# Kernel tuning notes

Measured on AMD Instinct MI355X. Metric: run time of the kernel, lower is better.

## Reference

```python
import jax, jax.numpy as jnp
import numpy as np

D = 256  # subgraph_width
N_CLASSES = 10
EPS = 1e-5  # torch LayerNorm default


def _layernorm(x, g, b):
    mu = jnp.mean(x, axis=-1, keepdims=True)
    var = jnp.var(x, axis=-1, keepdims=True)
    return (x - mu) * jax.lax.rsqrt(var + EPS) * g + b


def setup_inputs() -> dict:
    key = jax.random.key(0)
    ks = jax.random.split(key, 16)
    B, T, N = 64, 512, 512
    traj = jax.random.normal(ks[0], (B, T, 2), dtype=jnp.float32)
    labels = jax.random.randint(ks[1], (B,), 0, N_CLASSES)
    h = jax.random.normal(ks[2], (B, N, D), dtype=jnp.float32)
    valid_len = jnp.maximum(jax.random.randint(ks[3], (B,), 0, N), 1)
    s = 0.02
    params = dict(
        emb=jax.random.normal(ks[4], (N_CLASSES, D), dtype=jnp.float32) * s,
        w_mlp=jax.random.normal(ks[5], (2, D), dtype=jnp.float32) * s,
        b_mlp=jnp.zeros((D,), jnp.float32),
        ln_g=jnp.ones((D,), jnp.float32),
        ln_b=jnp.zeros((D,), jnp.float32),
        wq=jax.random.normal(ks[6], (D, D), dtype=jnp.float32) * s,
        bq=jnp.zeros((D,), jnp.float32),
        wk=jax.random.normal(ks[7], (D, D), dtype=jnp.float32) * s,
        bk=jnp.zeros((D,), jnp.float32),
        wv=jax.random.normal(ks[8], (D, D), dtype=jnp.float32) * s,
        bv=jnp.zeros((D,), jnp.float32),
        w_out=jax.random.normal(ks[9], (D, 1), dtype=jnp.float32) * s,
        b_out=jnp.zeros((1,), jnp.float32),
    )
    return dict(traj=traj, labels=labels, h=h, valid_len=valid_len, **params)


def reference(traj, labels, h, valid_len, emb, w_mlp, b_mlp, ln_g, ln_b,
              wq, bq, wk, bk, wv, bv, w_out, b_out):
    # MLP(in=2, out=D, activation='leaky'): Linear -> LayerNorm -> LeakyReLU
    x = jax.nn.leaky_relu(_layernorm(traj @ w_mlp + b_mlp, ln_g, ln_b))  # [B,T,D]
    le = emb[labels]                          # [B,D]
    x = x + le[:, None, :]                    # embed-add
    # SelfAttentionWithKeyFCLayer: Q from x, K/V from h, scaled, key-masked by valid_len
    q = x @ wq + bq                            # [B,T,D]
    k = h @ wk + bk                            # [B,N,D]
    v = h @ wv + bv                            # [B,N,D]
    scores = jnp.einsum('btd,bnd->btn', q, k) / jnp.sqrt(jnp.float32(D))
    N = h.shape[1]
    key_mask = jnp.arange(N)[None, :] < valid_len[:, None]          # [B,N]
    scores = jnp.where(key_mask[:, None, :], scores, jnp.float32(-1e9))
    attn = jax.nn.softmax(scores, axis=-1)
    enc = jnp.einsum('btn,bnd->btd', attn, v)  # [B,T,D]
    pooled = jnp.max(enc, axis=1) + le          # [B,D]
    return jax.nn.sigmoid(pooled @ w_out + b_out)  # [B,1]
```

## Files before the change

### kernel.cpp

```cpp
#include <hip/hip_runtime.h>
#include <math.h>

typedef float f32x4 __attribute__((ext_vector_type(4)));
typedef __bf16 bf16x8 __attribute__((ext_vector_type(8)));
typedef unsigned short u16x8 __attribute__((ext_vector_type(8)));
typedef unsigned short u16x4 __attribute__((ext_vector_type(4)));
typedef unsigned int u32x4 __attribute__((ext_vector_type(4)));

#define MFMA(a, b, c) __builtin_amdgcn_mfma_f32_16x16x32_bf16((a), (b), (c), 0, 0, 0)

static __device__ __forceinline__ unsigned short f2bf(float f) {
  unsigned u = __float_as_uint(f);
  u += 0x7FFFu + ((u >> 16) & 1u);
  return (unsigned short)(u >> 16);
}
static __device__ __forceinline__ float bf2f(unsigned short s) {
  return __uint_as_float(((unsigned)s) << 16);
}
static __device__ __forceinline__ unsigned pack2bf(float lo, float hi) {
  return (unsigned)f2bf(lo) | ((unsigned)f2bf(hi) << 16);
}

static __device__ __forceinline__ int swz512(int row, int col) {
  return row * 512 + (col ^ ((((row & 7) ^ (col >> 6)) & 7) << 4));
}
static __device__ __forceinline__ int swzV(int d, int col) {
  return d * 64 + (col ^ (((d >> 1) & 3) << 4));
}
static __device__ __forceinline__ int swzO(int d, int col) {
  return d * 256 + (col ^ ((((d & 7) ^ (col >> 7)) & 7) << 4));
}

static __device__ __forceinline__ void barp() {
  __builtin_amdgcn_sched_barrier(0);
  asm volatile("s_waitcnt lgkmcnt(0)");
  __builtin_amdgcn_s_barrier();
  __builtin_amdgcn_sched_barrier(0);
}

__global__ __launch_bounds__(256) void setup(
    const float* __restrict__ w0m, const float* __restrict__ w1m, const float* __restrict__ w2m,
    unsigned short* __restrict__ t0m, unsigned short* __restrict__ t1m, unsigned short* __restrict__ t2m,
    const float* __restrict__ w_mlp, const float* __restrict__ b_mlp, float* __restrict__ lnsc,
    const int* __restrict__ vlen, int* __restrict__ tasktab) {
  int bid = blockIdx.x;
  int t = threadIdx.x;
  if (bid == 48) {
    float w0 = w_mlp[t], w1 = w_mlp[256 + t], bb = b_mlp[t];
    float v[9] = {w0, w1, bb, w0 * w0, w1 * w1, w0 * w1, w0 * bb, w1 * bb, bb * bb};
    __shared__ float red[4][9];
#pragma unroll
    for (int j = 0; j < 9; ++j) {
      float s = v[j];
#pragma unroll
      for (int off = 32; off >= 1; off >>= 1) s += __shfl_xor(s, off, 64);
      v[j] = s;
    }
    if ((t & 63) == 0)
      for (int j = 0; j < 9; ++j) red[t >> 6][j] = v[j];
    __syncthreads();
    if (t < 9) lnsc[t] = red[0][t] + red[1][t] + red[2][t] + red[3][t];
    return;
  }
  if (bid == 49) {
    __shared__ int srank[64];
    if (t < 64) {
      int vb = vlen[t], r = 0;
      for (int j = 0; j < 64; ++j) {
        int vj = vlen[j];
        r += (vj > vb) || (vj == vb && j < t);
      }
      srank[r] = t;
    }
    __syncthreads();
    if (t < 64) {
      int r = t, b = srank[r];
      int xcd = r & 7, a = r >> 3;
      for (int tt = 0; tt < 4; ++tt)
        tasktab[(a * 4 + tt) * 8 + xcd] = (b << 2) | tt;
    }
    return;
  }
  int m = bid >> 4, t16 = bid & 15;
  const float* w = (m == 0) ? w0m : (m == 1) ? w1m : w2m;
  unsigned short* o = (m == 0) ? t0m : (m == 1) ? t1m : t2m;
  __shared__ float sm[64][65];
  int bi = t16 >> 2, bj = t16 & 3;
  for (int kb = 0; kb < 16; ++kb) {
    int idx = kb * 256 + t;
    int r = idx >> 6, c = idx & 63;
    sm[r][c] = w[(bi * 64 + r) * 256 + bj * 64 + c];
  }
  __syncthreads();
  for (int kb = 0; kb < 16; ++kb) {
    int idx = kb * 256 + t;
    int r = idx >> 6, c = idx & 63;
    int d = bj * 64 + r, e = bi * 64 + c;
    o[(e >> 5) * 8192 + d * 32 + (e & 31)] = f2bf(sm[c][r]);
  }
}

static __device__ __forceinline__ void issueB(u16x8* rr, const unsigned short* __restrict__ src,
                                              int tid) {
#pragma unroll
  for (int i = 0; i < 4; ++i) rr[i] = *(const u16x8*)(src + (size_t)(tid + 256 * i) * 8);
}
static __device__ __forceinline__ void writeB(const u16x8* rr, char* Bdst, int tid) {
#pragma unroll
  for (int i = 0; i < 4; ++i) {
    int idx = tid + 256 * i;
    *(u16x8*)(Bdst + swzV(idx >> 2, (idx & 3) * 16)) = rr[i];
  }
}
#define RS(i) (((i) % 3 == 0) ? r0 : ((i) % 3 == 1) ? r1 : r2)

static __device__ __forceinline__ void gemm_pipe(
    const unsigned short* __restrict__ Bpk, const unsigned short* Alds, unsigned short* Bbuf,
    int tid, int w, int g, int c15, u16x8 (&r0)[4], u16x8 (&r1)[4], u16x8 (&r2)[4],
    f32x4 (&acc)[4][4]) {
  writeB(r0, (char*)Bbuf, tid);
  barp();
#pragma unroll
  for (int c = 0; c < 8; ++c) {
    if (c + 2 < 8) issueB(RS(c + 2), Bpk + (size_t)(c + 2) * 8192, tid);
    const char* Bcur = (const char*)Bbuf + (c & 1) * 16384;
    bf16x8 af[4], bfv[4];
#pragma unroll
    for (int at = 0; at < 4; ++at)
      af[at] = *(const bf16x8*)((char*)Alds + swz512(at * 16 + c15, c * 64 + 16 * g));
#pragma unroll
    for (int nt = 0; nt < 4; ++nt)
      bfv[nt] = *(const bf16x8*)(Bcur + swzV(w * 64 + nt * 16 + c15, 16 * g));
    __builtin_amdgcn_s_setprio(1);
#pragma unroll
    for (int at = 0; at < 4; ++at)
#pragma unroll
      for (int nt = 0; nt < 4; ++nt) acc[at][nt] = MFMA(af[at], bfv[nt], acc[at][nt]);
    __builtin_amdgcn_s_setprio(0);
    if (c + 1 < 8) writeB(RS(c + 1), (char*)Bbuf + ((c + 1) & 1) * 16384, tid);
    barp();
  }
}

__global__ __launch_bounds__(256, 2) void gemms(
    const float* __restrict__ traj, const int* __restrict__ labels, const float* __restrict__ emb,
    const float* __restrict__ w_mlp, const float* __restrict__ b_mlp,
    const float* __restrict__ ln_g, const float* __restrict__ ln_b,
    const float* __restrict__ lnsc, const unsigned short* __restrict__ wqPk,
    const float* __restrict__ bq, unsigned short* __restrict__ q,
    const float* __restrict__ h, const int* __restrict__ vlen,
    const unsigned short* __restrict__ wkPk, const float* __restrict__ bk,
    const unsigned short* __restrict__ wvPk, const float* __restrict__ bv,
    unsigned short* __restrict__ kout, unsigned short* __restrict__ vT) {
  __shared__ unsigned short Alds[64 * 256];
  __shared__ unsigned short Bbuf[2 * 8192];
  int tid = threadIdx.x, w = tid >> 6, lane = tid & 63, g = lane >> 4, c15 = lane & 15;
  int bid = blockIdx.x;
  u16x8 r0[4], r1[4], r2[4];
  f32x4 acc[4][4];
#pragma unroll
  for (int a = 0; a < 4; ++a)
#pragma unroll
    for (int n = 0; n < 4; ++n) acc[a][n] = (f32x4){0.f, 0.f, 0.f, 0.f};

  if (bid < 512) {
    int tile = bid, b = tile >> 3;
    issueB(r0, wqPk, tid);
    issueB(r1, wqPk + 8192, tid);
    {
      int rrow = tid >> 5, cb = (tid & 31) * 8;
      int lab = labels[b];
      f32x4 wa0 = *(const f32x4*)(w_mlp + cb), wa1 = *(const f32x4*)(w_mlp + cb + 4);
      f32x4 wb0 = *(const f32x4*)(w_mlp + 256 + cb), wb1 = *(const f32x4*)(w_mlp + 256 + cb + 4);
      f32x4 bm0 = *(const f32x4*)(b_mlp + cb), bm1 = *(const f32x4*)(b_mlp + cb + 4);
      f32x4 g0 = *(const f32x4*)(ln_g + cb), g1 = *(const f32x4*)(ln_g + cb + 4);
      f32x4 lb0 = *(const f32x4*)(ln_b + cb), lb1 = *(const f32x4*)(ln_b + cb + 4);
      f32x4 le0 = *(const f32x4*)(emb + lab * 256 + cb), le1 = *(const f32x4*)(emb + lab * 256 + cb + 4);
      float s0 = lnsc[0], s1 = lnsc[1], s2 = lnsc[2], s3 = lnsc[3], s4 = lnsc[4],
            s5 = lnsc[5], s6 = lnsc[6], s7 = lnsc[7], s8 = lnsc[8];
#pragma unroll
      for (int i = 0; i < 8; ++i) {
        int row = i * 8 + rrow, grow = tile * 64 + row;
        float t0 = traj[grow * 2], t1 = traj[grow * 2 + 1];
        float mu = (t0 * s0 + t1 * s1 + s2) * (1.f / 256.f);
        float ea2 = (t0 * t0 * s3 + t1 * t1 * s4 + s8 +
                     2.f * (t0 * t1 * s5 + t0 * s6 + t1 * s7)) * (1.f / 256.f);
        float rstd = rsqrtf(ea2 - mu * mu + 1e-5f);
        u16x8 pk;
#pragma unroll
        for (int j = 0; j < 4; ++j) {
          float a0 = t0 * wa0[j] + t1 * wb0[j] + bm0[j];
          float y0 = (a0 - mu) * rstd * g0[j] + lb0[j];
          pk[j] = f2bf((y0 > 0.f ? y0 : 0.01f * y0) + le0[j]);
          float a1 = t0 * wa1[j] + t1 * wb1[j] + bm1[j];
          float y1 = (a1 - mu) * rstd * g1[j] + lb1[j];
          pk[j + 4] = f2bf((y1 > 0.f ? y1 : 0.01f * y1) + le1[j]);
        }
        *(u16x8*)((char*)Alds + swz512(row, cb * 2)) = pk;
      }
    }
    gemm_pipe(wqPk, Alds, Bbuf, tid, w, g, c15, r0, r1, r2, acc);
#pragma unroll
    for (int at = 0; at < 4; ++at)
#pragma unroll
      for (int nt = 0; nt < 4; ++nt) {
        int col = w * 64 + nt * 16 + c15;
        float bb = bq[col];
#pragma unroll
        for (int r = 0; r < 4; ++r)
          *(unsigned short*)((char*)Alds + swz512(at * 16 + 4 * g + r, col * 2)) =
              f2bf(acc[at][nt][r] + bb);
      }
    __syncthreads();
    {
      int row = tid >> 2;
      for (int i = 0; i < 8; ++i) {
        int colb = (tid & 3) * 128 + i * 16;
        u16x8 vv = *(const u16x8*)((char*)Alds + swz512(row, colb));
        *(u16x8*)(q + (size_t)(tile * 64 + row) * 256 + colb / 2) = vv;
      }
    }
    return;
  }

  bool is_k = (bid < 1024);
  int tile = bid - (is_k ? 512 : 1024);
  int b = tile >> 3;
  int nbase = (tile & 7) * 64;
  if (nbase >= vlen[b]) return;
  {
    const float* hb = h + (size_t)tile * 16384;
    f32x4 ha[8], hc[8];
#pragma unroll
    for (int i = 0; i < 8; ++i) {
      ha[i] = *(const f32x4*)(hb + i * 2048 + tid * 8);
      hc[i] = *(const f32x4*)(hb + i * 2048 + tid * 8 + 4);
    }
    const unsigned short* Bpk = is_k ? wkPk : wvPk;
    issueB(r0, Bpk, tid);
    issueB(r1, Bpk + 8192, tid);
#pragma unroll
    for (int i = 0; i < 8; ++i) {
      u16x8 pk;
#pragma unroll
      for (int j = 0; j < 4; ++j) { pk[j] = f2bf(ha[i][j]); pk[j + 4] = f2bf(hc[i][j]); }
      *(u16x8*)((char*)Alds + swz512(i * 8 + (tid >> 5), (tid & 31) * 16)) = pk;
    }
  }
  if (is_k) {
    gemm_pipe(wkPk, Alds, Bbuf, tid, w, g, c15, r0, r1, r2, acc);
#pragma unroll
    for (int at = 0; at < 4; ++at)
#pragma unroll
      for (int nt = 0; nt < 4; ++nt) {
        int col = w * 64 + nt * 16 + c15;
        float bb = bk[col];
#pragma unroll
        for (int r = 0; r < 4; ++r)
          *(unsigned short*)((char*)Alds + swz512(at * 16 + 4 * g + r, col * 2)) =
              f2bf(acc[at][nt][r] + bb);
      }
    __syncthreads();
    {
      int row = tid >> 2;
      for (int i = 0; i < 8; ++i) {
        int colb = (tid & 3) * 128 + i * 16;
        u16x8 vv = *(const u16x8*)((char*)Alds + swz512(row, colb));
        *(u16x8*)(kout + (size_t)(tile * 64 + row) * 256 + colb / 2) = vv;
      }
    }
  } else {
    gemm_pipe(wvPk, Alds, Bbuf, tid, w, g, c15, r0, r1, r2, acc);
#pragma unroll
    for (int at = 0; at < 4; ++at)
#pragma unroll
      for (int nt = 0; nt < 4; ++nt) {
        int col = w * 64 + nt * 16 + c15;
        float bb = bv[col];
        u16x4 o;
#pragma unroll
        for (int r = 0; r < 4; ++r) o[r] = f2bf(acc[at][nt][r] + bb);
        *(u16x4*)(vT + (size_t)b * 131072 + (size_t)col * 512 + nbase + at * 16 + 4 * g) = o;
      }
  }
}

__global__ __launch_bounds__(512) void attn(
    const unsigned short* __restrict__ q, const unsigned short* __restrict__ k,
    const unsigned short* __restrict__ vT, const int* __restrict__ valid_len,
    const int* __restrict__ tasktab, float* __restrict__ partial) {
  __shared__ unsigned short buf[2][16384];

  int task = tasktab[blockIdx.x];
  int b = task >> 2, tt = task & 3;
  int tid = threadIdx.x, w = tid >> 6, lane = tid & 63, g = lane >> 4, c15 = lane & 15;
  int vl = valid_len[b];
  int nit = (vl + 31) >> 5;

  bf16x8 qf[8];
  size_t qrow = (size_t)b * 512 + tt * 128 + w * 16 + c15;
#pragma unroll
  for (int kk = 0; kk < 8; ++kk)
    qf[kk] = *(const bf16x8*)(q + qrow * 256 + kk * 32 + 8 * g);

  f32x4 acco[16];
#pragma unroll
  for (int i = 0; i < 16; ++i) acco[i] = (f32x4){0.f, 0.f, 0.f, 0.f};
  float rs = 0.f;

  const unsigned short* kbase = k + (size_t)b * 512 * 256;
  const unsigned short* vbase = vT + (size_t)b * 131072;
  u16x8 kpre[2], vpre[2];

#pragma unroll
  for (int i = 0; i < 2; ++i) {
    int idx = tid + 512 * i, key = idx >> 5, s = idx & 31;
    kpre[i] = *(const u16x8*)(kbase + (size_t)key * 256 + s * 8);
  }
#pragma unroll
  for (int i = 0; i < 2; ++i) {
    int idx = tid + 512 * i, d = idx >> 2, s = idx & 3;
    vpre[i] = *(const u16x8*)(vbase + (size_t)d * 512 + s * 8);
  }
#pragma unroll
  for (int i = 0; i < 2; ++i) {
    int idx = tid + 512 * i, key = idx >> 5, s = idx & 31;
    *(u16x8*)((char*)buf[0] + swz512(key, s * 16)) = kpre[i];
  }
#pragma unroll
  for (int i = 0; i < 2; ++i) {
    int idx = tid + 512 * i, d = idx >> 2, s = idx & 3;
    *(u16x8*)((char*)(buf[0] + 8192) + swzV(d, s * 16)) = vpre[i];
  }

  for (int it = 0; it < nit; ++it) {
    int cur = it & 1;
    __syncthreads();
    bool pf = (it + 1 < nit);
    if (pf) {
      int n1 = (it + 1) * 32;
#pragma unroll
      for (int i = 0; i < 2; ++i) {
        int idx = tid + 512 * i, key = idx >> 5, s = idx & 31;
        kpre[i] = *(const u16x8*)(kbase + (size_t)(n1 + key) * 256 + s * 8);
      }
#pragma unroll
      for (int i = 0; i < 2; ++i) {
        int idx = tid + 512 * i, d = idx >> 2, s = idx & 3;
        vpre[i] = *(const u16x8*)(vbase + (size_t)d * 512 + n1 + s * 8);
      }
    }
    unsigned short* Klds = buf[cur];
    unsigned short* Vlds = buf[cur] + 8192;
    int n0 = it * 32;

    float p[2][4];
    unsigned u01[2], u23[2];
#pragma unroll
    for (int c = 0; c < 2; ++c) {
      f32x4 s4 = (f32x4){0.f, 0.f, 0.f, 0.f};
      __builtin_amdgcn_s_setprio(1);
#pragma unroll
      for (int kk = 0; kk < 8; ++kk) {
        bf16x8 kf = *(const bf16x8*)((char*)Klds + swz512(c * 16 + c15, kk * 64 + 16 * g));
        s4 = MFMA(kf, qf[kk], s4);
      }
      __builtin_amdgcn_s_setprio(0);
#pragma unroll
      for (int r = 0; r < 4; ++r) {
        int key = n0 + c * 16 + 4 * g + r;
        float pv = (key < vl) ? __expf(s4[r] * 0.0625f) : 0.f;
        p[c][r] = pv;
        rs += pv;
      }
      u01[c] = pack2bf(p[c][0], p[c][1]);
      u23[c] = pack2bf(p[c][2], p[c][3]);
    }
    int srcA = c15 | ((lane & 16) << 1);
    int srcB = srcA + 16;
    unsigned x0a = (unsigned)__shfl((int)u01[0], srcA, 64);
    unsigned x1a = (unsigned)__shfl((int)u01[1], srcA, 64);
    unsigned x0b = (unsigned)__shfl((int)u23[0], srcA, 64);
    unsigned x1b = (unsigned)__shfl((int)u23[1], srcA, 64);
    unsigned x0c = (unsigned)__shfl((int)u01[0], srcB, 64);
    unsigned x1c = (unsigned)__shfl((int)u01[1], srcB, 64);
    unsigned x0d = (unsigned)__shfl((int)u23[0], srcB, 64);
    unsigned x1d = (unsigned)__shfl((int)u23[1], srcB, 64);
    bool hi = g >= 2;
    union { u32x4 u; bf16x8 v; } pa;
    pa.u[0] = hi ? x1a : x0a;
    pa.u[1] = hi ? x1b : x0b;
    pa.u[2] = hi ? x1c : x0c;
    pa.u[3] = hi ? x1d : x0d;
    __builtin_amdgcn_s_setprio(1);
#pragma unroll
    for (int dt = 0; dt < 16; ++dt) {
      bf16x8 vf = *(const bf16x8*)((char*)Vlds + swzV(dt * 16 + c15, 16 * g));
      acco[dt] = MFMA(vf, pa.v, acco[dt]);
    }
    __builtin_amdgcn_s_setprio(0);
    if (pf) {
      unsigned short* Kn = buf[cur ^ 1];
      unsigned short* Vn = buf[cur ^ 1] + 8192;
#pragma unroll
      for (int i = 0; i < 2; ++i) {
        int idx = tid + 512 * i, key = idx >> 5, s = idx & 31;
        *(u16x8*)((char*)Kn + swz512(key, s * 16)) = kpre[i];
      }
#pragma unroll
      for (int i = 0; i < 2; ++i) {
        int idx = tid + 512 * i, d = idx >> 2, s = idx & 3;
        *(u16x8*)((char*)Vn + swzV(d, s * 16)) = vpre[i];
      }
    }
  }
  rs += __shfl_xor(rs, 16, 64);
  rs += __shfl_xor(rs, 32, 64);
  float inv = 1.f / rs;
  __syncthreads();
  int qcol = w * 16 + c15;
#pragma unroll
  for (int dt = 0; dt < 16; ++dt)
#pragma unroll
    for (int r = 0; r < 4; ++r) {
      int d = dt * 16 + 4 * g + r;
      *(unsigned short*)((char*)buf + swzO(d, qcol * 2)) = f2bf(acco[dt][r] * inv);
    }
  __syncthreads();
  {
    int d = tid & 255, half = tid >> 8;
    float m = -1e30f;
    for (int i = 0; i < 8; ++i) {
      u16x8 vv = *(const u16x8*)((char*)buf + swzO(d, half * 128 + i * 16));
#pragma unroll
      for (int j = 0; j < 8; ++j) m = fmaxf(m, bf2f(vv[j]));
    }
    partial[(((size_t)b * 4 + tt) * 2 + half) * 256 + d] = m;
  }
}

__global__ __launch_bounds__(256) void finalize(
    const float* __restrict__ partial, const float* __restrict__ emb,
    const int* __restrict__ labels, const float* __restrict__ w_out,
    const float* __restrict__ b_out, float* __restrict__ out) {
  int b = blockIdx.x, t = threadIdx.x;
  float m = -1e30f;
#pragma unroll
  for (int s8 = 0; s8 < 8; ++s8)
    m = fmaxf(m, partial[((size_t)b * 8 + s8) * 256 + t]);
  m += emb[labels[b] * 256 + t];
  __shared__ float red[256];
  red[t] = m * w_out[t];
  __syncthreads();
  for (int s = 128; s > 0; s >>= 1) {
    if (t < s) red[t] += red[t + s];
    __syncthreads();
  }
  if (t == 0) out[b] = 1.f / (1.f + __expf(-(red[0] + b_out[0])));
}

extern "C" void kernel_launch(void* const* d_in, const int* in_sizes, int n_in,
                              void* d_out, int out_size, void* d_ws, size_t ws_size,
                              hipStream_t stream) {
  const float* traj   = (const float*)d_in[0];
  const int*   labels = (const int*)d_in[1];
  const float* h      = (const float*)d_in[2];
  const int*   vlen   = (const int*)d_in[3];
  const float* emb    = (const float*)d_in[4];
  const float* w_mlp  = (const float*)d_in[5];
  const float* b_mlp  = (const float*)d_in[6];
  const float* ln_g   = (const float*)d_in[7];
  const float* ln_b   = (const float*)d_in[8];
  const float* wq     = (const float*)d_in[9];
  const float* bq     = (const float*)d_in[10];
  const float* wk     = (const float*)d_in[11];
  const float* bk     = (const float*)d_in[12];
  const float* wv     = (const float*)d_in[13];
  const float* bv     = (const float*)d_in[14];
  const float* w_out  = (const float*)d_in[15];
  const float* b_out  = (const float*)d_in[16];
  float* out = (float*)d_out;

  unsigned short* qb   = (unsigned short*)d_ws;
  unsigned short* kb   = qb + (size_t)32768 * 256;
  unsigned short* vT   = kb + (size_t)32768 * 256;
  unsigned short* wqPk = vT + (size_t)32768 * 256;
  unsigned short* wkPk = wqPk + 65536;
  unsigned short* wvPk = wkPk + 65536;
  float* lnsc    = (float*)(wvPk + 65536);
  float* partial = lnsc + 16;
  int*   tasktab = (int*)(partial + 64 * 8 * 256);

  setup<<<50, 256, 0, stream>>>(wq, wk, wv, wqPk, wkPk, wvPk, w_mlp, b_mlp, lnsc,
                                vlen, tasktab);
  gemms<<<1536, 256, 0, stream>>>(traj, labels, emb, w_mlp, b_mlp, ln_g, ln_b,
                                  lnsc, wqPk, bq, qb, h, vlen, wkPk, bk, wvPk, bv,
                                  kb, vT);
  attn<<<256, 512, 0, stream>>>(qb, kb, vT, vlen, tasktab, partial);
  finalize<<<64, 256, 0, stream>>>(partial, emb, labels, w_out, b_out, out);
}
```

Measured before the change: 82.59 us.

## Fuse K and V projections per tile and read weights directly from global

Drops the LDS double-buffered weight pipeline and has each wave load its B fragments straight from the pre-packed global weights, which are small and likely cache-resident. K and V projections now share one block per h tile, so the h tile is loaded and converted to bf16 once instead of twice, and the grid shrinks from 1536 to 1024 blocks. Removing the B buffer frees LDS, so launch bounds rise to 4 blocks per CU. The trade-off is that global/L2 fragment loads now sit directly in front of the MFMAs with no prefetch, and each block does twice as much serial work.

Result: faster. 76.83 us (-7.0%).

```diff
diff --git a/kernel.cpp b/kernel.cpp
--- a/kernel.cpp
+++ b/kernel.cpp
@@ -29,13 +29,6 @@
 }
 static __device__ __forceinline__ int swzO(int d, int col) {
   return d * 256 + (col ^ ((((d & 7) ^ (col >> 7)) & 7) << 4));
-}
-
-static __device__ __forceinline__ void barp() {
-  __builtin_amdgcn_sched_barrier(0);
-  asm volatile("s_waitcnt lgkmcnt(0)");
-  __builtin_amdgcn_s_barrier();
-  __builtin_amdgcn_sched_barrier(0);
 }
 
 __global__ __launch_bounds__(256) void setup(
@@ -100,49 +93,30 @@
   }
 }
 
-static __device__ __forceinline__ void issueB(u16x8* rr, const unsigned short* __restrict__ src,
-                                              int tid) {
-#pragma unroll
-  for (int i = 0; i < 4; ++i) rr[i] = *(const u16x8*)(src + (size_t)(tid + 256 * i) * 8);
-}
-static __device__ __forceinline__ void writeB(const u16x8* rr, char* Bdst, int tid) {
-#pragma unroll
-  for (int i = 0; i < 4; ++i) {
-    int idx = tid + 256 * i;
-    *(u16x8*)(Bdst + swzV(idx >> 2, (idx & 3) * 16)) = rr[i];
-  }
-}
-#define RS(i) (((i) % 3 == 0) ? r0 : ((i) % 3 == 1) ? r1 : r2)
-
-static __device__ __forceinline__ void gemm_pipe(
-    const unsigned short* __restrict__ Bpk, const unsigned short* Alds, unsigned short* Bbuf,
-    int tid, int w, int g, int c15, u16x8 (&r0)[4], u16x8 (&r1)[4], u16x8 (&r2)[4],
-    f32x4 (&acc)[4][4]) {
-  writeB(r0, (char*)Bbuf, tid);
-  barp();
+static __device__ __forceinline__ void gemm_direct(
+    const unsigned short* __restrict__ Bpk, const unsigned short* Alds,
+    int w, int g, int c15, f32x4 (&acc)[4][4]) {
+  const unsigned short* bp = Bpk + (w * 64 + c15) * 32 + 8 * g;
 #pragma unroll
   for (int c = 0; c < 8; ++c) {
-    if (c + 2 < 8) issueB(RS(c + 2), Bpk + (size_t)(c + 2) * 8192, tid);
-    const char* Bcur = (const char*)Bbuf + (c & 1) * 16384;
-    bf16x8 af[4], bfv[4];
+    bf16x8 bfv[4];
+#pragma unroll
+    for (int nt = 0; nt < 4; ++nt)
+      bfv[nt] = *(const bf16x8*)(bp + c * 8192 + nt * 512);
+    bf16x8 af[4];
 #pragma unroll
     for (int at = 0; at < 4; ++at)
       af[at] = *(const bf16x8*)((char*)Alds + swz512(at * 16 + c15, c * 64 + 16 * g));
-#pragma unroll
-    for (int nt = 0; nt < 4; ++nt)
-      bfv[nt] = *(const bf16x8*)(Bcur + swzV(w * 64 + nt * 16 + c15, 16 * g));
     __builtin_amdgcn_s_setprio(1);
 #pragma unroll
     for (int at = 0; at < 4; ++at)
 #pragma unroll
       for (int nt = 0; nt < 4; ++nt) acc[at][nt] = MFMA(af[at], bfv[nt], acc[at][nt]);
     __builtin_amdgcn_s_setprio(0);
-    if (c + 1 < 8) writeB(RS(c + 1), (char*)Bbuf + ((c + 1) & 1) * 16384, tid);
-    barp();
-  }
-}
-
-__global__ __launch_bounds__(256, 2) void gemms(
+  }
+}
+
+__global__ __launch_bounds__(256, 4) void gemms(
     const float* __restrict__ traj, const int* __restrict__ labels, const float* __restrict__ emb,
     const float* __restrict__ w_mlp, const float* __restrict__ b_mlp,
     const float* __restrict__ ln_g, const float* __restrict__ ln_b,
@@ -153,20 +127,12 @@
     const unsigned short* __restrict__ wvPk, const float* __restrict__ bv,
     unsigned short* __restrict__ kout, unsigned short* __restrict__ vT) {
   __shared__ unsigned short Alds[64 * 256];
-  __shared__ unsigned short Bbuf[2 * 8192];
   int tid = threadIdx.x, w = tid >> 6, lane = tid & 63, g = lane >> 4, c15 = lane & 15;
   int bid = blockIdx.x;
-  u16x8 r0[4], r1[4], r2[4];
   f32x4 acc[4][4];
-#pragma unroll
-  for (int a = 0; a < 4; ++a)
-#pragma unroll
-    for (int n = 0; n < 4; ++n) acc[a][n] = (f32x4){0.f, 0.f, 0.f, 0.f};
 
   if (bid < 512) {
     int tile = bid, b = tile >> 3;
-    issueB(r0, wqPk, tid);
-    issueB(r1, wqPk + 8192, tid);
     {
       int rrow = tid >> 5, cb = (tid & 31) * 8;
       int lab = labels[b];
@@ -199,7 +165,13 @@
         *(u16x8*)((char*)Alds + swz512(row, cb * 2)) = pk;
       }
     }
-    gemm_pipe(wqPk, Alds, Bbuf, tid, w, g, c15, r0, r1, r2, acc);
+#pragma unroll
+    for (int a = 0; a < 4; ++a)
+#pragma unroll
+      for (int n = 0; n < 4; ++n) acc[a][n] = (f32x4){0.f, 0.f, 0.f, 0.f};
+    __syncthreads();
+    gemm_direct(wqPk, Alds, w, g, c15, acc);
+    __syncthreads();
 #pragma unroll
     for (int at = 0; at < 4; ++at)
 #pragma unroll
@@ -223,8 +195,7 @@
     return;
   }
 
-  bool is_k = (bid < 1024);
-  int tile = bid - (is_k ? 512 : 1024);
+  int tile = bid - 512;
   int b = tile >> 3;
   int nbase = (tile & 7) * 64;
   if (nbase >= vlen[b]) return;
@@ -236,9 +207,6 @@
       ha[i] = *(const f32x4*)(hb + i * 2048 + tid * 8);
       hc[i] = *(const f32x4*)(hb + i * 2048 + tid * 8 + 4);
     }
-    const unsigned short* Bpk = is_k ? wkPk : wvPk;
-    issueB(r0, Bpk, tid);
-    issueB(r1, Bpk + 8192, tid);
 #pragma unroll
     for (int i = 0; i < 8; ++i) {
       u16x8 pk;
@@ -247,41 +215,50 @@
       *(u16x8*)((char*)Alds + swz512(i * 8 + (tid >> 5), (tid & 31) * 16)) = pk;
     }
   }
-  if (is_k) {
-    gemm_pipe(wkPk, Alds, Bbuf, tid, w, g, c15, r0, r1, r2, acc);
-#pragma unroll
-    for (int at = 0; at < 4; ++at)
-#pragma unroll
-      for (int nt = 0; nt < 4; ++nt) {
-        int col = w * 64 + nt * 16 + c15;
-        float bb = bk[col];
-#pragma unroll
-        for (int r = 0; r < 4; ++r)
-          *(unsigned short*)((char*)Alds + swz512(at * 16 + 4 * g + r, col * 2)) =
-              f2bf(acc[at][nt][r] + bb);
-      }
-    __syncthreads();
-    {
-      int row = tid >> 2;
-      for (int i = 0; i < 8; ++i) {
-        int colb = (tid & 3) * 128 + i * 16;
-        u16x8 vv = *(const u16x8*)((char*)Alds + swz512(row, colb));
-        *(u16x8*)(kout + (size_t)(tile * 64 + row) * 256 + colb / 2) = vv;
-      }
-    }
-  } else {
-    gemm_pipe(wvPk, Alds, Bbuf, tid, w, g, c15, r0, r1, r2, acc);
-#pragma unroll
-    for (int at = 0; at < 4; ++at)
-#pragma unroll
-      for (int nt = 0; nt < 4; ++nt) {
-        int col = w * 64 + nt * 16 + c15;
-        float bb = bv[col];
-        u16x4 o;
-#pragma unroll
-        for (int r = 0; r < 4; ++r) o[r] = f2bf(acc[at][nt][r] + bb);
-        *(u16x4*)(vT + (size_t)b * 131072 + (size_t)col * 512 + nbase + at * 16 + 4 * g) = o;
-      }
+#pragma unroll
+  for (int a = 0; a < 4; ++a)
+#pragma unroll
+    for (int n = 0; n < 4; ++n) acc[a][n] = (f32x4){0.f, 0.f, 0.f, 0.f};
+  __syncthreads();
+
+  gemm_direct(wvPk, Alds, w, g, c15, acc);
+#pragma unroll
+  for (int at = 0; at < 4; ++at)
+#pragma unroll
+    for (int nt = 0; nt < 4; ++nt) {
+      int col = w * 64 + nt * 16 + c15;
+      float bb = bv[col];
+      u16x4 o;
+#pragma unroll
+      for (int r = 0; r < 4; ++r) o[r] = f2bf(acc[at][nt][r] + bb);
+      *(u16x4*)(vT + (size_t)b * 131072 + (size_t)col * 512 + nbase + at * 16 + 4 * g) = o;
+    }
+
+#pragma unroll
+  for (int a = 0; a < 4; ++a)
+#pragma unroll
+    for (int n = 0; n < 4; ++n) acc[a][n] = (f32x4){0.f, 0.f, 0.f, 0.f};
+  gemm_direct(wkPk, Alds, w, g, c15, acc);
+  __syncthreads();
+#pragma unroll
+  for (int at = 0; at < 4; ++at)
+#pragma unroll
+    for (int nt = 0; nt < 4; ++nt) {
+      int col = w * 64 + nt * 16 + c15;
+      float bb = bk[col];
+#pragma unroll
+      for (int r = 0; r < 4; ++r)
+        *(unsigned short*)((char*)Alds + swz512(at * 16 + 4 * g + r, col * 2)) =
+            f2bf(acc[at][nt][r] + bb);
+    }
+  __syncthreads();
+  {
+    int row = tid >> 2;
+    for (int i = 0; i < 8; ++i) {
+      int colb = (tid & 3) * 128 + i * 16;
+      u16x8 vv = *(const u16x8*)((char*)Alds + swz512(row, colb));
+      *(u16x8*)(kout + (size_t)(tile * 64 + row) * 256 + colb / 2) = vv;
+    }
   }
 }
 
@@ -493,7 +470,7 @@
 
   setup<<<50, 256, 0, stream>>>(wq, wk, wv, wqPk, wkPk, wvPk, w_mlp, b_mlp, lnsc,
                                 vlen, tasktab);
-  gemms<<<1536, 256, 0, stream>>>(traj, labels, emb, w_mlp, b_mlp, ln_g, ln_b,
+  gemms<<<1024, 256, 0, stream>>>(traj, labels, emb, w_mlp, b_mlp, ln_g, ln_b,
                                   lnsc, wqPk, bq, qb, h, vlen, wkPk, bk, wvPk, bv,
                                   kb, vT);
   attn<<<256, 512, 0, stream>>>(qb, kb, vT, vlen, tasktab, partial);
```
